# Kernel optimization log

Measured on AMD Instinct MI355X. Metric: run time of the kernel, lower is better.

Reference implementation:

```python
import jax, jax.numpy as jnp
import numpy as np

N = 100000   # nodes
E = 500000   # edges
D = 128      # node_hidden_size
ED = 128     # edge_emb_dim
L = 8        # n_message_passes
H = 4        # num_heads
V = 8192     # node_vocab_size
G = 64       # num_graphs
A = 100      # num_actions
NFLOW = 8
NPOS = 64


def setup_inputs() -> dict:
    key = jax.random.key(0)
    ks = jax.random.split(key, 24)
    rn = lambda k, shape, s: jax.random.normal(k, shape, jnp.float32) * s
    inp = {}
    # graph tensors
    inp['x'] = jax.random.randint(ks[0], (N,), 0, V)
    inp['node_type'] = jax.random.randint(ks[1], (N,), 0, 2)
    inp['batch'] = jnp.sort(jax.random.randint(ks[2], (N,), 0, G))
    inp['edge_index'] = jax.random.randint(ks[3], (2, E), 0, N)
    inp['flow'] = jax.random.randint(ks[4], (E,), 0, NFLOW)
    inp['position'] = jax.random.randint(ks[5], (E,), 0, NPOS)
    inp['block'] = jax.random.randint(ks[6], (N,), 0, 4096)
    inp['num_graphs'] = G
    # parameters
    sd = 1.0 / np.sqrt(D)
    se = 1.0 / np.sqrt(ED)
    inp['emb_table'] = rn(ks[7], (V, D), 1.0)
    inp['flow_emb'] = rn(ks[8], (NFLOW, ED), 1.0)
    inp['pos_emb'] = rn(ks[9], (NPOS, ED), 1.0)
    inp['blk_emb'] = rn(ks[10], (2, ED), 1.0)
    inp['Wq'] = rn(ks[11], (L, D, D), sd)
    inp['Wk'] = rn(ks[12], (L, D, D), sd)
    inp['Wv'] = rn(ks[13], (L, D, D), sd)
    inp['Wek'] = rn(ks[14], (L, ED, D), se)
    inp['Wev'] = rn(ks[15], (L, ED, D), se)
    inp['Wo'] = rn(ks[16], (L, D, D), sd)
    inp['Weu'] = rn(ks[17], (L, 2 * D + ED, ED), 1.0 / np.sqrt(2 * D + ED))
    inp['QW1'] = rn(ks[18], (D + ED, D), 1.0 / np.sqrt(D + ED))
    inp['Qb1'] = jnp.zeros((D,), jnp.float32)
    inp['QW2'] = rn(ks[19], (D, A), sd)
    inp['Qb2'] = jnp.zeros((A,), jnp.float32)
    return inp


def _forward(x, node_type, batch, edge_index, flow, position, block, num_graphs,
             emb_table, flow_emb, pos_emb, blk_emb,
             Wq, Wk, Wv, Wek, Wev, Wo, Weu, QW1, Qb1, QW2, Qb2):
    src, dst = edge_index[0], edge_index[1]
    feat = emb_table[x]                                        # [N, D]
    # EdgeEncoding: flow-type + position embeddings + block-crossing indicator
    crossing = (block[src] != block[dst]).astype(jnp.int32)
    e = flow_emb[flow] + pos_emb[position] + blk_emb[crossing]  # [E, ED]

    Nn, Dd = feat.shape
    dh = Dd // H
    scale = 1.0 / np.sqrt(dh)
    n_layers = Wq.shape[0]
    for l in range(n_layers):
        q = (feat @ Wq[l]).reshape(Nn, H, dh)
        k = (feat @ Wk[l]).reshape(Nn, H, dh)
        v = (feat @ Wv[l]).reshape(Nn, H, dh)
        ek = (e @ Wek[l]).reshape(-1, H, dh)
        ev = (e @ Wev[l]).reshape(-1, H, dh)
        # per-edge attention logits, softmax over edges sharing a dst node
        scores = jnp.sum(q[dst] * (k[src] + ek), axis=-1) * scale  # [E, H]
        m = jax.lax.stop_gradient(
            jax.ops.segment_max(scores, dst, num_segments=Nn))
        ex = jnp.exp(scores - m[dst])
        den = jax.ops.segment_sum(ex, dst, num_segments=Nn)
        alpha = ex / (den[dst] + 1e-16)                            # [E, H]
        msg = alpha[..., None] * (v[src] + ev)                     # [E, H, dh]
        agg = jax.ops.segment_sum(msg, dst, num_segments=Nn).reshape(Nn, Dd)
        feat_new = jax.nn.relu(feat + agg @ Wo[l])
        e = jax.nn.relu(e + jnp.concatenate([feat[src], feat[dst], e], axis=-1) @ Weu[l])
        feat = feat_new

    # scatter_mean over instruction nodes (type == 0) per graph
    maskf = (node_type == 0).astype(feat.dtype)
    ncnt = jax.ops.segment_sum(maskf, batch, num_segments=num_graphs)
    gagg = jax.ops.segment_sum(feat * maskf[:, None], batch, num_segments=num_graphs)
    gagg = gagg / jnp.maximum(ncnt, 1.0)[:, None]
    # scatter_mean of edge features per graph (edge's graph = graph of its src node)
    eb = batch[src]
    ecnt = jax.ops.segment_sum(jnp.ones((e.shape[0],), e.dtype), eb, num_segments=num_graphs)
    eagg = jax.ops.segment_sum(e, eb, num_segments=num_graphs)
    eagg = eagg / jnp.maximum(ecnt, 1.0)[:, None]

    ga = jnp.concatenate([gagg, eagg], axis=-1)                    # [G, D+ED]
    h = jax.nn.relu(ga @ QW1 + Qb1)
    logits = h @ QW2 + Qb2
    return jax.nn.log_softmax(logits, axis=-1)


def reference(x, node_type, batch, edge_index, flow, position, block, num_graphs,
              emb_table, flow_emb, pos_emb, blk_emb,
              Wq, Wk, Wv, Wek, Wev, Wo, Weu, QW1, Qb1, QW2, Qb2):
    return _forward(x, node_type, batch, edge_index, flow, position, block,
                    int(num_graphs), emb_table, flow_emb, pos_emb, blk_emb,
                    Wq, Wk, Wv, Wek, Wev, Wo, Weu, QW1, Qb1, QW2, Qb2)
```

## Files before the change

### kernel.cpp

```cpp
#include <hip/hip_runtime.h>
#include <stdint.h>

#define NN 100000
#define NE 500000
#define DD 128
#define NL 8
#define NG 64
#define NA 100
#define DET_PAIRS 65536

typedef unsigned short u16;
typedef unsigned int u32;
typedef __attribute__((ext_vector_type(8))) short short8;
typedef __attribute__((ext_vector_type(4))) float f32x4;

union U4 { uint4 v; u16 s[8]; };

__device__ __forceinline__ float b2f(u16 u){ union{u32 i; float f;} x; x.i=((u32)u)<<16; return x.f; }
__device__ __forceinline__ u16 f2b(float f){ union{float f; u32 i;} x; x.f=f; u32 b=x.i; b += 0x7fffu + ((b>>16)&1u); return (u16)(b>>16); }

__global__ void zero_k(int* __restrict__ p, int n){
  int i = blockIdx.x*256 + threadIdx.x;
  if (i < n) p[i] = 0;
}
__global__ void diag_k(u16* __restrict__ out, int n, float val){
  int i = blockIdx.x*256 + threadIdx.x;
  if (i < n) out[i] = f2b(val);
}

__global__ void detect_k(const u16* __restrict__ raw, int* __restrict__ flags){
  int i = blockIdx.x*256 + threadIdx.x;
  int ok = 0;
  if (i < DET_PAIRS){
    u16 v = raw[2*i];
    int e = (v>>7)&0xFF;
    ok = ((e >= 107 && e <= 147) || ((v & 0x7FFFu) == 0)) ? 1 : 0;
  }
  unsigned long long b = __ballot(ok);
  if ((threadIdx.x & 63) == 0) atomicAdd(&flags[2], (int)__popcll(b));
}
__global__ void flagset_k(int* __restrict__ flags){
  if (threadIdx.x==0) flags[0] = (flags[2] < DET_PAIRS/2) ? 1 : 0;
}
__global__ void tobf16_k(const void* __restrict__ in, u16* __restrict__ out, int n,
                         const int* __restrict__ flags){
  int i = blockIdx.x*256 + threadIdx.x;
  if (i >= n) return;
  if (flags[0]) out[i] = f2b(((const float*)in)[i]);
  else          out[i] = ((const u16*)in)[i];
}
__global__ void convT_k(const void* __restrict__ in, u16* __restrict__ out, int L, int K, int Nn,
                        const int* __restrict__ flags){
  int id = blockIdx.x*256 + threadIdx.x;
  int tot = L*K*Nn;
  if (id >= tot) return;
  int l = id/(K*Nn); int r = id - l*K*Nn;
  int k = r/Nn; int n = r - k*Nn;
  u16 v;
  if (flags[0]) v = f2b(((const float*)in)[id]);
  else          v = ((const u16*)in)[id];
  out[(size_t)l*K*Nn + (size_t)n*K + k] = v;
}

__global__ void featinit_k(const int* __restrict__ x, const u16* __restrict__ emb, u16* __restrict__ feat){
  int id = blockIdx.x*256 + threadIdx.x;
  if (id >= NN*16) return;
  int row = id>>4, c8 = (id&15)*8;
  int g = x[row];
  *(uint4*)(feat + (size_t)row*DD + c8) = *(const uint4*)(emb + (size_t)g*DD + c8);
}

__global__ void count_k(const int* __restrict__ dst, int* __restrict__ cnt){
  int e = blockIdx.x*256 + threadIdx.x;
  if (e < NE) atomicAdd(&cnt[dst[e]], 1);
}
__global__ void scan1_k(const int* __restrict__ cnt, int* __restrict__ excl, int* __restrict__ bsum, int n){
  __shared__ int sh[256];
  int t = threadIdx.x, g = blockIdx.x*256 + t;
  int v = (g<n) ? cnt[g] : 0;
  sh[t] = v; __syncthreads();
  for (int d=1; d<256; d<<=1){
    int xv = (t>=d) ? sh[t-d] : 0;
    __syncthreads();
    sh[t] += xv;
    __syncthreads();
  }
  if (g<n) excl[g] = sh[t]-v;
  if (t==255) bsum[blockIdx.x] = sh[255];
}
__global__ void scan2_k(int* __restrict__ bsum, int nb){
  if (threadIdx.x==0 && blockIdx.x==0){
    int a=0;
    for (int i=0;i<nb;i++){ int x=bsum[i]; bsum[i]=a; a+=x; }
  }
}
__global__ void scan3_k(const int* __restrict__ excl, const int* __restrict__ bsum,
                        int* __restrict__ offs, int* __restrict__ cursor, int n, int total){
  int g = blockIdx.x*256 + threadIdx.x;
  if (g < n){ int o = excl[g] + bsum[g>>8]; offs[g]=o; cursor[g]=o; }
  if (g==0) offs[n] = total;
}
__global__ void fill_k(const int* __restrict__ dst, int* __restrict__ cursor, int* __restrict__ perm){
  int e = blockIdx.x*256 + threadIdx.x;
  if (e < NE){ int p = atomicAdd(&cursor[dst[e]], 1); perm[p] = e; }
}
__global__ void make_sorted_k(const int* __restrict__ perm, const int* __restrict__ src,
                              const int* __restrict__ dst, int* __restrict__ srcs, int* __restrict__ dsts){
  int i = blockIdx.x*256 + threadIdx.x;
  if (i < NE){ int ed = perm[i]; srcs[i] = src[ed]; dsts[i] = dst[ed]; }
}

__global__ void edgeinit_k(const int* __restrict__ perm, const int* __restrict__ flow,
                           const int* __restrict__ pos, const int* __restrict__ blk,
                           const int* __restrict__ srcs, const int* __restrict__ dsts,
                           const int* __restrict__ batch,
                           const u16* __restrict__ flow_emb, const u16* __restrict__ pos_emb,
                           const u16* __restrict__ blk_emb,
                           u16* __restrict__ e, int* __restrict__ ebgs){
  int id = blockIdx.x*256 + threadIdx.x;
  if (id >= NE*16) return;
  int i = id>>4, c8 = (id&15)*8;
  int ed = perm[i];
  int s = srcs[i], d = dsts[i];
  int cross = (blk[s] != blk[d]) ? 1 : 0;
  U4 a,b,c,o;
  a.v = *(const uint4*)(flow_emb + (size_t)flow[ed]*DD + c8);
  b.v = *(const uint4*)(pos_emb  + (size_t)pos[ed]*DD + c8);
  c.v = *(const uint4*)(blk_emb  + (size_t)cross*DD + c8);
  #pragma unroll
  for (int j=0;j<8;j++) o.s[j] = f2b(b2f(a.s[j]) + b2f(b.s[j]) + b2f(c.s[j]));
  *(uint4*)(e + (size_t)i*DD + c8) = o.v;
  if ((id&15)==0) ebgs[i] = batch[s];
}

__global__ __launch_bounds__(256,4) void gemm_k(
    const u16* A0, const int* __restrict__ i0,
    const u16* A1, const int* __restrict__ i1,
    const u16* A2, const int* __restrict__ i2, int nchunks,
    const u16* __restrict__ Bt, int Ktot,
    const u16* res, int do_relu, int res_lds,
    u16* C, int M)
{
  __shared__ u16 As[128*128];
  int t = threadIdx.x;
  int mbase = blockIdx.x*128;
  int lane = t & 63, w = t>>6;
  int wrow = (w>>1)*64, wcol = (w&1)*64;
  int rl_w = t>>4, gw = t&15;
  int l15 = lane & 15, quad = lane>>4;
  f32x4 acc[4][4];
  #pragma unroll
  for (int mi=0;mi<4;mi++)
    #pragma unroll
    for (int ni=0;ni<4;ni++){ acc[mi][ni][0]=0.f; acc[mi][ni][1]=0.f; acc[mi][ni][2]=0.f; acc[mi][ni][3]=0.f; }

  for (int c=0; c<nchunks; c++){
    const u16* A = (c==0)?A0:((c==1)?A1:A2);
    const int* idx = (c==0)?i0:((c==1)?i1:i2);
    if (c > 0) __syncthreads();
    #pragma unroll
    for (int i=0;i<8;i++){
      int gm = mbase + rl_w + 16*i;
      uint4 av = make_uint4(0u,0u,0u,0u);
      if (gm < M){
        size_t grow = idx ? (size_t)idx[gm] : (size_t)gm;
        av = *(const uint4*)(A + grow*DD + gw*8);
      }
      *(uint4*)(As + (size_t)(i*256 + rl_w*16 + (gw ^ rl_w))*8) = av;
    }
    __syncthreads();
    #pragma unroll
    for (int kk=0;kk<4;kk++){
      int kg = kk*4 + quad;
      short8 af[4], bfr[4];
      #pragma unroll
      for (int mi=0;mi<4;mi++)
        af[mi] = *(const short8*)(As + (size_t)(((wrow>>4)+mi)*256 + l15*16 + (kg ^ l15))*8);
      #pragma unroll
      for (int ni=0;ni<4;ni++)
        bfr[ni] = *(const short8*)(Bt + (size_t)(wcol + ni*16 + l15)*Ktot + c*128 + kg*8);
      #pragma unroll
      for (int mi=0;mi<4;mi++)
        #pragma unroll
        for (int ni=0;ni<4;ni++)
          acc[mi][ni] = __builtin_amdgcn_mfma_f32_16x16x32_bf16(af[mi], bfr[ni], acc[mi][ni], 0, 0, 0);
    }
  }

  if (res_lds){
    #pragma unroll
    for (int mi=0;mi<4;mi++){
      #pragma unroll
      for (int r4=0;r4<4;r4++){
        int row = wrow + mi*16 + quad*4 + r4;
        #pragma unroll
        for (int ni=0;ni<4;ni++){
          int col = wcol + ni*16 + l15;
          float r = b2f(As[(row>>4)*2048 + (row&15)*128 + (((col>>3) ^ (row&15))<<3) + (col&7)]);
          float vv = acc[mi][ni][r4] + r;
          if (do_relu && vv < 0.f) vv = 0.f;
          acc[mi][ni][r4] = vv;
        }
      }
    }
  }
  __syncthreads();
  #pragma unroll
  for (int mi=0;mi<4;mi++){
    #pragma unroll
    for (int r4=0;r4<4;r4++){
      int row = wrow + mi*16 + quad*4 + r4;
      #pragma unroll
      for (int ni=0;ni<4;ni++){
        int col = wcol + ni*16 + l15;
        As[row*128 + ((((col>>3) ^ (row&15))<<3)) + (col&7)] = f2b(acc[mi][ni][r4]);
      }
    }
  }
  __syncthreads();
  #pragma unroll
  for (int i=0;i<8;i++){
    int row = rl_w + 16*i;
    int gm = mbase + row;
    if (gm >= M) continue;
    U4 av; av.v = *(const uint4*)(As + row*128 + ((gw ^ (row&15))<<3));
    if (res_lds){
      *(uint4*)(C + (size_t)gm*DD + gw*8) = av.v;
      continue;
    }
    float vals[8];
    #pragma unroll
    for (int j=0;j<8;j++) vals[j] = b2f(av.s[j]);
    if (res){
      U4 rv; rv.v = *(const uint4*)(res + (size_t)gm*DD + gw*8);
      #pragma unroll
      for (int j=0;j<8;j++) vals[j] += b2f(rv.s[j]);
    }
    U4 ov;
    #pragma unroll
    for (int j=0;j<8;j++){
      float v = vals[j];
      if (do_relu && v < 0.f) v = 0.f;
      ov.s[j] = f2b(v);
    }
    *(uint4*)(C + (size_t)gm*DD + gw*8) = ov.v;
  }
}

__global__ __launch_bounds__(256,4) void scores_fused_k(
    const u16* __restrict__ E, const u16* __restrict__ WekT,
    const u16* __restrict__ q, const u16* __restrict__ k,
    const int* __restrict__ srcs, const int* __restrict__ dsts,
    float* __restrict__ sc)
{
  __shared__ u16 As[128*128];
  int t = threadIdx.x;
  int ebase = blockIdx.x*128;
  int lane = t & 63, w = t>>6;
  int wrow = (w>>1)*64, wcol = (w&1)*64;
  int rl_w = t>>4, gw = t&15;
  int l15 = lane & 15, quad = lane>>4;
  #pragma unroll
  for (int i=0;i<8;i++){
    int gm = ebase + rl_w + 16*i;
    uint4 av = make_uint4(0u,0u,0u,0u);
    if (gm < NE) av = *(const uint4*)(E + (size_t)gm*DD + gw*8);
    *(uint4*)(As + (size_t)(i*256 + rl_w*16 + (gw ^ rl_w))*8) = av;
  }
  __syncthreads();
  f32x4 acc[4][4];
  #pragma unroll
  for (int mi=0;mi<4;mi++)
    #pragma unroll
    for (int ni=0;ni<4;ni++){ acc[mi][ni][0]=0.f; acc[mi][ni][1]=0.f; acc[mi][ni][2]=0.f; acc[mi][ni][3]=0.f; }
  #pragma unroll
  for (int kk=0;kk<4;kk++){
    int kg = kk*4 + quad;
    short8 af[4], bfr[4];
    #pragma unroll
    for (int mi=0;mi<4;mi++)
      af[mi] = *(const short8*)(As + (size_t)(((wrow>>4)+mi)*256 + l15*16 + (kg ^ l15))*8);
    #pragma unroll
    for (int ni=0;ni<4;ni++)
      bfr[ni] = *(const short8*)(WekT + (size_t)(wcol + ni*16 + l15)*DD + kg*8);
    #pragma unroll
    for (int mi=0;mi<4;mi++)
      #pragma unroll
      for (int ni=0;ni<4;ni++)
        acc[mi][ni] = __builtin_amdgcn_mfma_f32_16x16x32_bf16(af[mi], bfr[ni], acc[mi][ni], 0, 0, 0);
  }
  __syncthreads();
  #pragma unroll
  for (int mi=0;mi<4;mi++){
    #pragma unroll
    for (int r4=0;r4<4;r4++){
      int row = wrow + mi*16 + quad*4 + r4;
      #pragma unroll
      for (int ni=0;ni<4;ni++){
        int col = wcol + ni*16 + l15;
        As[row*128 + ((((col>>3) ^ (row&15))<<3)) + (col&7)] = f2b(acc[mi][ni][r4]);
      }
    }
  }
  __syncthreads();
  const float scale = 0.17677669529663689f;
  for (int pid = t; pid < 512; pid += 256){
    int le = pid>>2, h = pid&3;
    int e = ebase + le;
    if (e >= NE) continue;
    int s = srcs[e], d = dsts[e];
    float dot = 0.f;
    #pragma unroll
    for (int j4=0;j4<4;j4++){
      int off = h*32 + j4*8;
      U4 qv, kv, ev;
      qv.v = *(const uint4*)(q + (size_t)d*DD + off);
      kv.v = *(const uint4*)(k + (size_t)s*DD + off);
      ev.v = *(const uint4*)(As + le*128 + ((((h*4+j4) ^ (le&15))<<3)));
      #pragma unroll
      for (int j=0;j<8;j++) dot += b2f(qv.s[j]) * (b2f(kv.s[j]) + b2f(ev.s[j]));
    }
    sc[(size_t)e*4 + h] = dot * scale;
  }
}

__global__ __launch_bounds__(256,2) void nodeagg_k(
    const float* __restrict__ sc, const u16* __restrict__ v,
    const u16* __restrict__ E, const int* __restrict__ srcs,
    const int* __restrict__ offs, const u16* __restrict__ WevL,
    u16* __restrict__ agg)
{
  __shared__ float sh[16*4*129];
  int t = threadIdx.x;
  int n16 = t>>4;
  int node = blockIdx.x*16 + n16;
  int sub = t & 15;
  int hown = sub>>2;
  int offc = sub*8;
  int beg = 0, end = 0;
  if (node < NN){ beg = offs[node]; end = offs[node+1]; }
  float m[4] = {-1e30f,-1e30f,-1e30f,-1e30f};
  float den[4] = {0.f,0.f,0.f,0.f};
  for (int i=beg;i<end;i++){
    float4 s4 = *(const float4*)(sc + (size_t)i*4);
    float ss[4] = {s4.x, s4.y, s4.z, s4.w};
    #pragma unroll
    for (int h=0;h<4;h++){
      float mn = fmaxf(m[h], ss[h]);
      den[h] = den[h]*__expf(m[h]-mn) + __expf(ss[h]-mn);
      m[h] = mn;
    }
  }
  float inv[4];
  #pragma unroll
  for (int h=0;h<4;h++) inv[h] = 1.0f/(den[h] + 1e-16f);
  float uh[4][8];
  #pragma unroll
  for (int h=0;h<4;h++)
    #pragma unroll
    for (int j=0;j<8;j++) uh[h][j]=0.f;
  float accv[8] = {0.f,0.f,0.f,0.f,0.f,0.f,0.f,0.f};
  for (int i=beg;i<end;i++){
    float4 s4 = *(const float4*)(sc + (size_t)i*4);
    float al[4] = { __expf(s4.x-m[0])*inv[0], __expf(s4.y-m[1])*inv[1],
                    __expf(s4.z-m[2])*inv[2], __expf(s4.w-m[3])*inv[3] };
    U4 ee; ee.v = *(const uint4*)(E + (size_t)i*DD + offc);
    #pragma unroll
    for (int j=0;j<8;j++){
      float ev = b2f(ee.s[j]);
      #pragma unroll
      for (int h=0;h<4;h++) uh[h][j] += al[h]*ev;
    }
    U4 vv; vv.v = *(const uint4*)(v + (size_t)srcs[i]*DD + offc);
    #pragma unroll
    for (int j=0;j<8;j++) accv[j] += al[hown]*b2f(vv.s[j]);
  }
  #pragma unroll
  for (int h=0;h<4;h++)
    #pragma unroll
    for (int j=0;j<8;j++) sh[(n16*4 + h)*129 + offc + j] = uh[h][j];
  __syncthreads();
  if (node >= NN) return;
  float o8[8];
  #pragma unroll
  for (int j=0;j<8;j++) o8[j] = accv[j];
  int base = (n16*4 + hown)*129;
  for (int kk=0;kk<128;kk+=4){
    float u0 = sh[base+kk], u1 = sh[base+kk+1], u2 = sh[base+kk+2], u3 = sh[base+kk+3];
    U4 w0,w1,w2,w3;
    w0.v = *(const uint4*)(WevL + (size_t)kk*DD + offc);
    w1.v = *(const uint4*)(WevL + (size_t)(kk+1)*DD + offc);
    w2.v = *(const uint4*)(WevL + (size_t)(kk+2)*DD + offc);
    w3.v = *(const uint4*)(WevL + (size_t)(kk+3)*DD + offc);
    #pragma unroll
    for (int j=0;j<8;j++)
      o8[j] += u0*b2f(w0.s[j]) + u1*b2f(w1.s[j]) + u2*b2f(w2.s[j]) + u3*b2f(w3.s[j]);
  }
  U4 o;
  #pragma unroll
  for (int j=0;j<8;j++) o.s[j] = f2b(o8[j]);
  *(uint4*)(agg + (size_t)node*DD + offc) = o.v;
}

__global__ void hist_k(const int* __restrict__ gid, const int* __restrict__ mask, int n,
                       int* __restrict__ hist){
  __shared__ int lh[NG];
  int t = threadIdx.x;
  if (t < NG) lh[t]=0;
  __syncthreads();
  int i = blockIdx.x*256 + t;
  if (i < n && (!mask || mask[i]==0)) atomicAdd(&lh[gid[i]], 1);
  __syncthreads();
  if (t < NG && lh[t]) atomicAdd(&hist[t], lh[t]);
}
__global__ void scan64_k(const int* __restrict__ hist, int* __restrict__ base, int* __restrict__ cur){
  if (threadIdx.x==0){
    int a=0;
    for (int g=0; g<NG; g++){ base[g]=a; cur[g]=a; a+=hist[g]; }
    base[NG]=a;
  }
}
__global__ void fillperm_k(const int* __restrict__ gid, const int* __restrict__ mask, int n,
                           int* __restrict__ cur, int* __restrict__ operm){
  __shared__ int lh[NG];
  __shared__ int lb[NG];
  int t = threadIdx.x;
  if (t < NG) lh[t]=0;
  __syncthreads();
  int i = blockIdx.x*256 + t;
  int g=-1, r=0;
  if (i < n && (!mask || mask[i]==0)){ g = gid[i]; r = atomicAdd(&lh[g], 1); }
  __syncthreads();
  if (t < NG && lh[t]) lb[t] = atomicAdd(&cur[t], lh[t]);
  __syncthreads();
  if (g >= 0) operm[lb[g] + r] = i;
}
__global__ __launch_bounds__(256,4) void poolsum_k(
    const u16* __restrict__ feat, const int* __restrict__ operm,
    const int* __restrict__ base, int chunks, float* __restrict__ outsum)
{
  __shared__ float sh[16*128];
  int g = blockIdx.x / chunks, c = blockIdx.x % chunks;
  int beg = base[g], end = base[g+1];
  int len = end - beg;
  int cb = beg + (int)(((long long)len*c)/chunks);
  int ce = beg + (int)(((long long)len*(c+1))/chunks);
  int t = threadIdx.x, grp = t>>4, sub = t&15;
  float acc[8] = {0.f,0.f,0.f,0.f,0.f,0.f,0.f,0.f};
  for (int i = cb+grp; i < ce; i += 16){
    int r = operm[i];
    U4 fv; fv.v = *(const uint4*)(feat + (size_t)r*DD + sub*8);
    #pragma unroll
    for (int j=0;j<8;j++) acc[j] += b2f(fv.s[j]);
  }
  #pragma unroll
  for (int j=0;j<8;j++) sh[grp*128 + sub*8 + j] = acc[j];
  __syncthreads();
  if (t < 128){
    float s = 0.f;
    #pragma unroll
    for (int r=0;r<16;r++) s += sh[r*128 + t];
    if (s != 0.f) atomicAdd(&outsum[g*DD + t], s);
  }
}

__global__ void ganorm_k(const float* __restrict__ gsum, const int* __restrict__ ncnt,
                         const float* __restrict__ esum, const int* __restrict__ ecnt,
                         float* __restrict__ ga){
  int id = blockIdx.x*256 + threadIdx.x;
  if (id >= NG*256) return;
  int g = id>>8, c = id&255;
  float v;
  if (c < 128) v = gsum[g*DD + c] / fmaxf((float)ncnt[g], 1.f);
  else         v = esum[g*DD + (c-128)] / fmaxf((float)ecnt[g], 1.f);
  ga[(size_t)g*256 + c] = v;
}

__global__ void mlp1_k(const float* __restrict__ ga, const u16* __restrict__ QW1,
                       const u16* __restrict__ Qb1, float* __restrict__ h){
  int o = blockIdx.x*256 + threadIdx.x;
  if (o >= NG*DD) return;
  int g = o>>7, j = o&127;
  float s = b2f(Qb1[j]);
  #pragma unroll 4
  for (int kq=0;kq<256;kq++) s += ga[(size_t)g*256 + kq] * b2f(QW1[(size_t)kq*DD + j]);
  h[o] = fmaxf(s, 0.f);
}

__global__ __launch_bounds__(128) void mlp2_k(const float* __restrict__ h, const u16* __restrict__ QW2,
                       const u16* __restrict__ Qb2, void* __restrict__ out, const int* __restrict__ flags){
  __shared__ float lsh[NA];
  __shared__ float red[128];
  int g = blockIdx.x, t = threadIdx.x;
  float s = -1e30f;
  if (t < NA){
    float acc = b2f(Qb2[t]);
    #pragma unroll 4
    for (int kq=0;kq<DD;kq++) acc += h[(size_t)g*DD + kq] * b2f(QW2[(size_t)kq*NA + t]);
    lsh[t] = acc; s = acc;
  }
  red[t] = s; __syncthreads();
  for (int d=64; d>0; d>>=1){ if (t<d) red[t] = fmaxf(red[t], red[t+d]); __syncthreads(); }
  float m = red[0]; __syncthreads();
  float ex = (t < NA) ? __expf(lsh[t]-m) : 0.f;
  red[t] = ex; __syncthreads();
  for (int d=64; d>0; d>>=1){ if (t<d) red[t] += red[t+d]; __syncthreads(); }
  float lse = m + __logf(red[0]);
  if (t < NA){
    float r = lsh[t]-lse;
    if (flags[0]) ((float*)out)[(size_t)g*NA + t] = r;
    else          ((u16*)out)[(size_t)g*NA + t]  = f2b(r);
  }
}

extern "C" void kernel_launch(void* const* d_in, const int* in_sizes, int n_in,
                              void* d_out, int out_size, void* d_ws, size_t ws_size,
                              hipStream_t stream) {
  (void)in_sizes; (void)n_in;
  const int* x      = (const int*)d_in[0];
  const int* ntype  = (const int*)d_in[1];
  const int* batch  = (const int*)d_in[2];
  const int* eidx   = (const int*)d_in[3];
  const int* src    = eidx;
  const int* dstp   = eidx + NE;
  const int* flow   = (const int*)d_in[4];
  const int* pos    = (const int*)d_in[5];
  const int* blk    = (const int*)d_in[6];

  char* p = (char*)d_ws;
  auto alloc = [&](size_t bytes)->char* {
    char* r = p; p += (bytes + 255) & ~(size_t)255; return r;
  };
  u16* embB  = (u16*)alloc((size_t)8192*DD*2);
  u16* flowB = (u16*)alloc(8*DD*2);
  u16* posB  = (u16*)alloc(64*DD*2);
  u16* blkB  = (u16*)alloc(2*DD*2);
  const size_t WSZb = (size_t)NL*DD*DD*2;
  u16* WevB = (u16*)alloc(WSZb);
  u16* QW1B = (u16*)alloc((size_t)256*DD*2);
  u16* Qb1B = (u16*)alloc(DD*2);
  u16* QW2B = (u16*)alloc((size_t)DD*NA*2);
  u16* Qb2B = (u16*)alloc(NA*2);
  u16* WqT  = (u16*)alloc(WSZb);
  u16* WkT  = (u16*)alloc(WSZb);
  u16* WvT  = (u16*)alloc(WSZb);
  u16* WekT = (u16*)alloc(WSZb);
  u16* WoT  = (u16*)alloc(WSZb);
  u16* WeuT = (u16*)alloc((size_t)NL*DD*384*2);
  const size_t NB = (size_t)NN*DD*2;
  u16* A  = (u16*)alloc(NB);
  u16* QB = (u16*)alloc(NB);
  u16* KB = (u16*)alloc(NB);
  u16* SCRATCH = (u16*)alloc(NB);
  const size_t EB = (size_t)NE*DD*2;
  u16* E = (u16*)alloc(EB);
  float* scores = (float*)alloc((size_t)NE*4*4);
  int* srcs   = (int*)alloc((size_t)NE*4);
  int* dsts   = (int*)alloc((size_t)NE*4);
  int* ebgs   = (int*)alloc((size_t)NE*4);
  int* offs   = (int*)alloc((size_t)(NN+1)*4);
  float* gsum = (float*)alloc((size_t)NG*DD*4);
  float* esum = (float*)alloc((size_t)NG*DD*4);
  float* ga = (float*)alloc((size_t)NG*256*4);
  float* h  = (float*)alloc((size_t)NG*DD*4);
  int* flags = (int*)alloc(16);

  char* q = (char*)SCRATCH;
  auto suballoc = [&](size_t bytes)->char* {
    char* r = q; q += (bytes + 255) & ~(size_t)255; return r;
  };
  int* perm   = (int*)suballoc((size_t)NE*4);
  int* cnt    = (int*)suballoc((size_t)NN*4);
  int* excl   = (int*)suballoc((size_t)NN*4);
  int* bsum   = (int*)suballoc(1024*4);
  int* cursor = (int*)suballoc((size_t)NN*4);
  int* eperm  = (int*)suballoc((size_t)NE*4);
  int* nperm  = (int*)suballoc((size_t)NN*4);
  int* ehist  = (int*)suballoc(NG*4);
  int* ebase  = (int*)suballoc((NG+1)*4);
  int* ecur   = (int*)suballoc(NG*4);
  int* nhist  = (int*)suballoc(NG*4);
  int* nbase  = (int*)suballoc((NG+1)*4);
  int* ncur   = (int*)suballoc(NG*4);

  size_t needed = (size_t)(p - (char*)d_ws);
  if (needed > ws_size){
    diag_k<<<(out_size+255)/256,256,0,stream>>>((u16*)d_out, out_size, (float)(ws_size>>20));
    return;
  }

  zero_k<<<1,256,0,stream>>>(flags, 4);
  detect_k<<<(DET_PAIRS+255)/256,256,0,stream>>>((const u16*)d_in[8], flags);
  flagset_k<<<1,64,0,stream>>>(flags);
  auto conv = [&](int idx, u16* dst, int n){
    tobf16_k<<<(n+255)/256,256,0,stream>>>(d_in[idx], dst, n, flags);
  };
  auto convT = [&](int idx, u16* dst, int L, int K, int Nc){
    int n = L*K*Nc;
    convT_k<<<(n+255)/256,256,0,stream>>>(d_in[idx], dst, L, K, Nc, flags);
  };
  conv(8,  embB,  8192*DD);
  conv(9,  flowB, 8*DD);
  conv(10, posB,  64*DD);
  conv(11, blkB,  2*DD);
  convT(12, WqT,  NL, DD, DD);
  convT(13, WkT,  NL, DD, DD);
  convT(14, WvT,  NL, DD, DD);
  convT(15, WekT, NL, DD, DD);
  conv(16, WevB, NL*DD*DD);
  convT(17, WoT,  NL, DD, DD);
  convT(18, WeuT, NL, 384, DD);
  conv(19, QW1B, 256*DD);
  conv(20, Qb1B, DD);
  conv(21, QW2B, DD*NA);
  conv(22, Qb2B, NA);

  zero_k<<<(NN+255)/256,256,0,stream>>>(cnt, NN);
  count_k<<<(NE+255)/256,256,0,stream>>>(dstp, cnt);
  int nb = (NN+255)/256;
  scan1_k<<<nb,256,0,stream>>>(cnt, excl, bsum, NN);
  scan2_k<<<1,64,0,stream>>>(bsum, nb);
  scan3_k<<<nb,256,0,stream>>>(excl, bsum, offs, cursor, NN, NE);
  fill_k<<<(NE+255)/256,256,0,stream>>>(dstp, cursor, perm);
  make_sorted_k<<<(NE+255)/256,256,0,stream>>>(perm, src, dstp, srcs, dsts);
  featinit_k<<<(NN*16+255)/256,256,0,stream>>>(x, embB, A);
  edgeinit_k<<<(NE*16+255)/256,256,0,stream>>>(perm, flow, pos, blk, srcs, dsts, batch,
                                               flowB, posB, blkB, E, ebgs);

  dim3 gN((NN+127)/128), gE((NE+127)/128);
  for (int l=0; l<NL; l++){
    const u16* wq  = WqT  + (size_t)l*DD*DD;
    const u16* wk  = WkT  + (size_t)l*DD*DD;
    const u16* wv  = WvT  + (size_t)l*DD*DD;
    const u16* wek = WekT + (size_t)l*DD*DD;
    const u16* wo  = WoT  + (size_t)l*DD*DD;
    const u16* wevL= WevB + (size_t)l*DD*DD;
    const u16* weu = WeuT + (size_t)l*DD*384;

    gemm_k<<<gN,256,0,stream>>>(A,nullptr,nullptr,nullptr,nullptr,nullptr,1, wq,128, nullptr,0,0, QB, NN);
    gemm_k<<<gN,256,0,stream>>>(A,nullptr,nullptr,nullptr,nullptr,nullptr,1, wk,128, nullptr,0,0, KB, NN);
    scores_fused_k<<<gE,256,0,stream>>>(E, wek, QB, KB, srcs, dsts, scores);
    gemm_k<<<gN,256,0,stream>>>(A,nullptr,nullptr,nullptr,nullptr,nullptr,1, wv,128, nullptr,0,0, KB, NN);
    nodeagg_k<<<(NN+15)/16,256,0,stream>>>(scores, KB, E, srcs, offs, wevL, QB);
    gemm_k<<<gE,256,0,stream>>>(A,srcs, A,dsts, E,nullptr, 3, weu,384, nullptr,1,1, E, NE);
    gemm_k<<<gN,256,0,stream>>>(QB,nullptr,nullptr,nullptr,nullptr,nullptr,1, wo,128, A,1,0, A, NN);
  }

  zero_k<<<1,256,0,stream>>>(ehist, NG);
  zero_k<<<1,256,0,stream>>>(nhist, NG);
  zero_k<<<(NG*DD+255)/256,256,0,stream>>>((int*)gsum, NG*DD);
  zero_k<<<(NG*DD+255)/256,256,0,stream>>>((int*)esum, NG*DD);
  hist_k<<<(NE+255)/256,256,0,stream>>>(ebgs, nullptr, NE, ehist);
  hist_k<<<(NN+255)/256,256,0,stream>>>(batch, ntype, NN, nhist);
  scan64_k<<<1,64,0,stream>>>(ehist, ebase, ecur);
  scan64_k<<<1,64,0,stream>>>(nhist, nbase, ncur);
  fillperm_k<<<(NE+255)/256,256,0,stream>>>(ebgs, nullptr, NE, ecur, eperm);
  fillperm_k<<<(NN+255)/256,256,0,stream>>>(batch, ntype, NN, ncur, nperm);
  const int ECH = 16, NCH = 4;
  poolsum_k<<<NG*ECH,256,0,stream>>>(E, eperm, ebase, ECH, esum);
  poolsum_k<<<NG*NCH,256,0,stream>>>(A, nperm, nbase, NCH, gsum);
  ganorm_k<<<(NG*256+255)/256,256,0,stream>>>(gsum, nhist, esum, ehist, ga);
  mlp1_k<<<(NG*DD+255)/256,256,0,stream>>>(ga, QW1B, Qb1B, h);
  mlp2_k<<<NG,128,0,stream>>>(h, QW2B, Qb2B, d_out, flags);
}
```

Baseline: 4.544 ms.

## Fuse Q/K/V projections into one kernel and split softmax stats out of nodeagg

Replaces three separate node GEMM launches with a single qkv_k kernel that computes Q, K and V into separate buffers, with V going to the scratch buffer, which frees KB from being overwritten. The per-node softmax max and denominator pass moves into a separate lightweight mden_k kernel, one thread per node, so nodeagg_k no longer walks each edge list twice across 16 threads and can raise its occupancy hint from 2 to 4. Launch bounds for gemm_k and scores_fused_k go from 4 to 5 blocks per SM. The trade-offs are an extra kernel launch and a small mden buffer, plus possible register pressure at the higher occupancy targets. qkv_k still reloads the A tile from global memory for each of the three weights.

```diff
diff --git a/kernel.cpp b/kernel.cpp
--- a/kernel.cpp
+++ b/kernel.cpp
@@ -133,7 +133,7 @@
   if ((id&15)==0) ebgs[i] = batch[s];
 }
 
-__global__ __launch_bounds__(256,4) void gemm_k(
+__global__ __launch_bounds__(256,5) void gemm_k(
     const u16* A0, const int* __restrict__ i0,
     const u16* A1, const int* __restrict__ i1,
     const u16* A2, const int* __restrict__ i2, int nchunks,
@@ -247,7 +247,79 @@
   }
 }
 
-__global__ __launch_bounds__(256,4) void scores_fused_k(
+__global__ __launch_bounds__(256,5) void qkv_k(
+    const u16* __restrict__ A, const u16* __restrict__ B0,
+    const u16* __restrict__ B1, const u16* __restrict__ B2,
+    u16* __restrict__ C0, u16* __restrict__ C1, u16* __restrict__ C2, int M)
+{
+  __shared__ u16 As[128*128];
+  int t = threadIdx.x;
+  int mbase = blockIdx.x*128;
+  int lane = t & 63, w = t>>6;
+  int wrow = (w>>1)*64, wcol = (w&1)*64;
+  int rl_w = t>>4, gw = t&15;
+  int l15 = lane & 15, quad = lane>>4;
+  const u16* Bs_[3] = {B0,B1,B2};
+  u16* Cs_[3] = {C0,C1,C2};
+  for (int s=0;s<3;s++){
+    if (s>0) __syncthreads();
+    #pragma unroll
+    for (int i=0;i<8;i++){
+      int gm = mbase + rl_w + 16*i;
+      uint4 av = make_uint4(0u,0u,0u,0u);
+      if (gm < M) av = *(const uint4*)(A + (size_t)gm*DD + gw*8);
+      *(uint4*)(As + (size_t)(i*256 + rl_w*16 + (gw ^ rl_w))*8) = av;
+    }
+    __syncthreads();
+    const u16* Bt = Bs_[s];
+    f32x4 acc[4][4];
+    #pragma unroll
+    for (int mi=0;mi<4;mi++)
+      #pragma unroll
+      for (int ni=0;ni<4;ni++){ acc[mi][ni][0]=0.f; acc[mi][ni][1]=0.f; acc[mi][ni][2]=0.f; acc[mi][ni][3]=0.f; }
+    #pragma unroll
+    for (int kk=0;kk<4;kk++){
+      int kg = kk*4 + quad;
+      short8 af[4], bfr[4];
+      #pragma unroll
+      for (int mi=0;mi<4;mi++)
+        af[mi] = *(const short8*)(As + (size_t)(((wrow>>4)+mi)*256 + l15*16 + (kg ^ l15))*8);
+      #pragma unroll
+      for (int ni=0;ni<4;ni++)
+        bfr[ni] = *(const short8*)(Bt + (size_t)(wcol + ni*16 + l15)*DD + kg*8);
+      #pragma unroll
+      for (int mi=0;mi<4;mi++)
+        #pragma unroll
+        for (int ni=0;ni<4;ni++)
+          acc[mi][ni] = __builtin_amdgcn_mfma_f32_16x16x32_bf16(af[mi], bfr[ni], acc[mi][ni], 0, 0, 0);
+    }
+    __syncthreads();
+    #pragma unroll
+    for (int mi=0;mi<4;mi++){
+      #pragma unroll
+      for (int r4=0;r4<4;r4++){
+        int row = wrow + mi*16 + quad*4 + r4;
+        #pragma unroll
+        for (int ni=0;ni<4;ni++){
+          int col = wcol + ni*16 + l15;
+          As[row*128 + ((((col>>3) ^ (row&15))<<3)) + (col&7)] = f2b(acc[mi][ni][r4]);
+        }
+      }
+    }
+    __syncthreads();
+    u16* C = Cs_[s];
+    #pragma unroll
+    for (int i=0;i<8;i++){
+      int row = rl_w + 16*i;
+      int gm = mbase + row;
+      if (gm >= M) continue;
+      U4 av; av.v = *(const uint4*)(As + row*128 + ((gw ^ (row&15))<<3));
+      *(uint4*)(C + (size_t)gm*DD + gw*8) = av.v;
+    }
+  }
+}
+
+__global__ __launch_bounds__(256,5) void scores_fused_k(
     const u16* __restrict__ E, const u16* __restrict__ WekT,
     const u16* __restrict__ q, const u16* __restrict__ k,
     const int* __restrict__ srcs, const int* __restrict__ dsts,
@@ -324,8 +396,33 @@
   }
 }
 
-__global__ __launch_bounds__(256,2) void nodeagg_k(
-    const float* __restrict__ sc, const u16* __restrict__ v,
+__global__ void mden_k(const float* __restrict__ sc, const int* __restrict__ offs,
+                       float* __restrict__ mden){
+  int node = blockIdx.x*256 + threadIdx.x;
+  if (node >= NN) return;
+  int beg = offs[node], end = offs[node+1];
+  float m[4] = {-1e30f,-1e30f,-1e30f,-1e30f};
+  float den[4] = {0.f,0.f,0.f,0.f};
+  for (int i=beg;i<end;i++){
+    float4 s4 = *(const float4*)(sc + (size_t)i*4);
+    float ss[4] = {s4.x, s4.y, s4.z, s4.w};
+    #pragma unroll
+    for (int h=0;h<4;h++){
+      float mn = fmaxf(m[h], ss[h]);
+      den[h] = den[h]*__expf(m[h]-mn) + __expf(ss[h]-mn);
+      m[h] = mn;
+    }
+  }
+  float4 mv = make_float4(m[0],m[1],m[2],m[3]);
+  float4 iv = make_float4(1.f/(den[0]+1e-16f), 1.f/(den[1]+1e-16f),
+                          1.f/(den[2]+1e-16f), 1.f/(den[3]+1e-16f));
+  *(float4*)(mden + (size_t)node*8)     = mv;
+  *(float4*)(mden + (size_t)node*8 + 4) = iv;
+}
+
+__global__ __launch_bounds__(256,4) void nodeagg_k(
+    const float* __restrict__ sc, const float* __restrict__ mden,
+    const u16* __restrict__ v,
     const u16* __restrict__ E, const int* __restrict__ srcs,
     const int* __restrict__ offs, const u16* __restrict__ WevL,
     u16* __restrict__ agg)
@@ -338,22 +435,14 @@
   int hown = sub>>2;
   int offc = sub*8;
   int beg = 0, end = 0;
-  if (node < NN){ beg = offs[node]; end = offs[node+1]; }
-  float m[4] = {-1e30f,-1e30f,-1e30f,-1e30f};
-  float den[4] = {0.f,0.f,0.f,0.f};
-  for (int i=beg;i<end;i++){
-    float4 s4 = *(const float4*)(sc + (size_t)i*4);
-    float ss[4] = {s4.x, s4.y, s4.z, s4.w};
-    #pragma unroll
-    for (int h=0;h<4;h++){
-      float mn = fmaxf(m[h], ss[h]);
-      den[h] = den[h]*__expf(m[h]-mn) + __expf(ss[h]-mn);
-      m[h] = mn;
-    }
-  }
-  float inv[4];
-  #pragma unroll
-  for (int h=0;h<4;h++) inv[h] = 1.0f/(den[h] + 1e-16f);
+  float m[4] = {0,0,0,0}, inv[4] = {0,0,0,0};
+  if (node < NN){
+    beg = offs[node]; end = offs[node+1];
+    float4 mv = *(const float4*)(mden + (size_t)node*8);
+    float4 iv = *(const float4*)(mden + (size_t)node*8 + 4);
+    m[0]=mv.x; m[1]=mv.y; m[2]=mv.z; m[3]=mv.w;
+    inv[0]=iv.x; inv[1]=iv.y; inv[2]=iv.z; inv[3]=iv.w;
+  }
   float uh[4][8];
   #pragma unroll
   for (int h=0;h<4;h++)
@@ -555,6 +644,7 @@
   const size_t EB = (size_t)NE*DD*2;
   u16* E = (u16*)alloc(EB);
   float* scores = (float*)alloc((size_t)NE*4*4);
+  float* mden   = (float*)alloc((size_t)NN*8*4);
   int* srcs   = (int*)alloc((size_t)NE*4);
   int* dsts   = (int*)alloc((size_t)NE*4);
   int* ebgs   = (int*)alloc((size_t)NE*4);
@@ -565,6 +655,7 @@
   float* h  = (float*)alloc((size_t)NG*DD*4);
   int* flags = (int*)alloc(16);
 
+  u16* VB = SCRATCH;
   char* q = (char*)SCRATCH;
   auto suballoc = [&](size_t bytes)->char* {
     char* r = q; q += (bytes + 255) & ~(size_t)255; return r;
@@ -637,11 +728,10 @@
     const u16* wevL= WevB + (size_t)l*DD*DD;
     const u16* weu = WeuT + (size_t)l*DD*384;
 
-    gemm_k<<<gN,256,0,stream>>>(A,nullptr,nullptr,nullptr,nullptr,nullptr,1, wq,128, nullptr,0,0, QB, NN);
-    gemm_k<<<gN,256,0,stream>>>(A,nullptr,nullptr,nullptr,nullptr,nullptr,1, wk,128, nullptr,0,0, KB, NN);
+    qkv_k<<<gN,256,0,stream>>>(A, wq, wk, wv, QB, KB, VB, NN);
     scores_fused_k<<<gE,256,0,stream>>>(E, wek, QB, KB, srcs, dsts, scores);
-    gemm_k<<<gN,256,0,stream>>>(A,nullptr,nullptr,nullptr,nullptr,nullptr,1, wv,128, nullptr,0,0, KB, NN);
-    nodeagg_k<<<(NN+15)/16,256,0,stream>>>(scores, KB, E, srcs, offs, wevL, QB);
+    mden_k<<<(NN+255)/256,256,0,stream>>>(scores, offs, mden);
+    nodeagg_k<<<(NN+15)/16,256,0,stream>>>(scores, mden, VB, E, srcs, offs, wevL, QB);
     gemm_k<<<gE,256,0,stream>>>(A,srcs, A,dsts, E,nullptr, 3, weu,384, nullptr,1,1, E, NE);
     gemm_k<<<gN,256,0,stream>>>(QB,nullptr,nullptr,nullptr,nullptr,nullptr,1, wo,128, A,1,0, A, NN);
   }
```

Measured after the change: 8.711 ms. 1.92x slower.
